# Kernel tuning notes

Hardware: AMD Instinct MI355X
Metric: run time of the kernel (lower is better)

Reference implementation:

```python
import jax, jax.numpy as jnp
import numpy as np

B, N = 2, 6
C_IN, C_MID = 512, 512
D, C_OUT = 112, 80
OGH, OGW, DS = 256, 704, 16
FH, FW = OGH // DS, OGW // DS  # 16, 44
D_MIN, D_MAX = 2.0, 58.0
NX, NY, NZ = 128, 128, 1
VSIZE = np.array([0.8, 0.8, 8.0], dtype=np.float32)
VCOORD = np.array([-51.2 + 0.4, -51.2 + 0.4, -5.0 + 4.0], dtype=np.float32)


def make_frustum():
    # (D, FH, FW, 4) with entries (x_pix, y_pix, depth, 1)
    ones = jnp.ones((D, FH, FW), jnp.float32)
    d = jnp.linspace(D_MIN, D_MAX, D)[:, None, None] * jnp.ones((1, FH, FW))
    x = jnp.linspace(0.0, OGW - 1.0, FW)[None, None, :] * jnp.ones((D, FH, 1))
    y = jnp.linspace(0.0, OGH - 1.0, FH)[None, :, None] * jnp.ones((D, 1, FW))
    return jnp.stack([x, y, d, ones], axis=-1)


def setup_inputs() -> dict:
    key = jax.random.key(0)
    ks = jax.random.split(key, 24)
    eye = jnp.eye(4, dtype=jnp.float32)
    K = jnp.array([[1266.0, 0.0, 800.0, 0.0],
                   [0.0, 1266.0, 450.0, 0.0],
                   [0.0, 0.0, 1.0, 0.0],
                   [0.0, 0.0, 0.0, 1.0]], jnp.float32)
    inp = {
        'feat': jax.random.normal(ks[0], (B * N, C_IN, FH, FW), jnp.float32),
        'w1': 0.05 * jax.random.normal(ks[1], (C_MID, C_IN, 3, 3), jnp.float32),
        'g1': 1.0 + 0.1 * jax.random.normal(ks[2], (C_MID,), jnp.float32),
        'b1': 0.1 * jax.random.normal(ks[3], (C_MID,), jnp.float32),
        'm1': 0.1 * jax.random.normal(ks[4], (C_MID,), jnp.float32),
        'v1': 0.5 + jax.random.uniform(ks[5], (C_MID,), jnp.float32),
        'w2': 0.05 * jax.random.normal(ks[6], (C_MID, C_MID, 3, 3), jnp.float32),
        'g2': 1.0 + 0.1 * jax.random.normal(ks[7], (C_MID,), jnp.float32),
        'b2': 0.1 * jax.random.normal(ks[8], (C_MID,), jnp.float32),
        'm2': 0.1 * jax.random.normal(ks[9], (C_MID,), jnp.float32),
        'v2': 0.5 + jax.random.uniform(ks[10], (C_MID,), jnp.float32),
        'w_out': 0.05 * jax.random.normal(ks[11], (D + C_OUT, C_MID, 1, 1), jnp.float32),
        'b_out': 0.1 * jax.random.normal(ks[12], (D + C_OUT,), jnp.float32),
        'sensor2ego': eye + 0.05 * jax.random.normal(ks[13], (B, N, 4, 4), jnp.float32),
        'sensor2virtual': eye + 0.05 * jax.random.normal(ks[14], (B, N, 4, 4), jnp.float32),
        'intrin': K + 0.01 * jax.random.normal(ks[15], (B, N, 4, 4), jnp.float32),
        'ida': eye + 0.01 * jax.random.normal(ks[16], (B, N, 4, 4), jnp.float32),
        'ref_heights': 1.5 + 0.2 * jax.random.normal(ks[17], (B, N), jnp.float32),
        'bda': eye + 0.01 * jax.random.normal(ks[18], (B, 4, 4), jnp.float32),
    }
    return inp


def _conv(x, w, p):
    return jax.lax.conv_general_dilated(x, w, (1, 1), [(p, p), (p, p)],
                                         dimension_numbers=('NCHW', 'OIHW', 'NCHW'))


def _bn(x, g, b, m, v):
    s = (g / jnp.sqrt(v + 1e-5))
    return (x - m[None, :, None, None]) * s[None, :, None, None] + b[None, :, None, None]


def get_geometry(sensor2ego, sensor2virtual, intrin, ida, ref_heights, bda):
    frustum = make_frustum()[..., None]  # (D,FH,FW,4,1)
    pts = jnp.linalg.inv(ida)[:, :, None, None, None] @ frustum  # (B,N,D,FH,FW,4,1)
    ref = ref_heights[:, :, None, None, None, None]
    height = -pts[..., 2, :] + ref  # (B,N,D,FH,FW,1)
    pc = pts.at[..., 2, :].set(10.0)
    pc = jnp.concatenate([pc[..., :2, :] * pc[..., 2:3, :], pc[..., 2:, :]], axis=-2)
    cv = sensor2virtual @ jnp.linalg.inv(intrin)
    pv = cv[:, :, None, None, None] @ pc
    ratio = height[..., 0] / pv[..., 1, 0]  # (B,N,D,FH,FW)
    pts = pv * ratio[..., None, None]
    pts = pts.at[..., 3, :].set(1.0)
    ce = sensor2ego @ jnp.linalg.inv(sensor2virtual)
    pts = ce[:, :, None, None, None] @ pts
    pts = (bda[:, None, None, None, None] @ pts)[..., 0]
    return pts[..., :3]  # (B,N,D,FH,FW,3)


def reference(feat, w1, g1, b1, m1, v1, w2, g2, b2, m2, v2, w_out, b_out,
              sensor2ego, sensor2virtual, intrin, ida, ref_heights, bda):
    # DepthNet head
    h = jax.nn.relu(_bn(_conv(feat, w1, 1), g1, b1, m1, v1))
    h = jax.nn.relu(_bn(_conv(h, w2, 1), g2, b2, m2, v2))
    hf = _conv(h, w_out, 0) + b_out[None, :, None, None]  # (B*N, D+C, FH, FW)
    depth = jax.nn.softmax(hf[:, :D], axis=1).reshape(B, N, D, FH, FW)
    context = hf[:, D:].reshape(B, N, C_OUT, FH, FW)

    geom = get_geometry(sensor2ego, sensor2virtual, intrin, ida, ref_heights, bda)

    # voxel indices
    vsize = jnp.asarray(VSIZE)
    vcoord = jnp.asarray(VCOORD)
    idx = ((geom - (vcoord - vsize / 2.0)) / vsize).astype(jnp.int32)
    valid = (jnp.all(idx >= 0, axis=-1) & (idx[..., 0] < NX)
             & (idx[..., 1] < NY) & (idx[..., 2] < NZ))

    # LSS outer product: (B,N,D,FH,FW,C)
    vol = jnp.einsum('bndhw,bnchw->bndhwc', depth, context)
    YX = NY * NX
    sid = idx[..., 1] * NX + idx[..., 0] + jnp.arange(B, dtype=jnp.int32)[:, None, None, None, None] * YX
    sid = jnp.where(valid, sid, B * YX).reshape(-1)
    bev = jax.ops.segment_sum(vol.reshape(-1, C_OUT), sid, num_segments=B * YX + 1)[:B * YX]
    return bev.reshape(B, NY, NX, C_OUT).transpose(0, 3, 1, 2)  # (B,C,NY,NX)
```

## Files before the change

kernel.cpp:

```cpp
#include <hip/hip_runtime.h>
#include <stdint.h>

#define NB   2
#define NN   6
#define NIMG 12
#define CIN  512
#define CMID 512
#define DD   112
#define COUT 80
#define FHh  16
#define FWw  44
#define NPIX 704
#define NPOS 8448
#define KK   4608
#define NXg  128
#define NYg  128
#define YX   16384
#define MAT_STRIDE 56
#define PADPIX 828
#define PROW 46

typedef short short8 __attribute__((ext_vector_type(8)));
typedef float f32x4  __attribute__((ext_vector_type(4)));

#define GLD16(g, l) __builtin_amdgcn_global_load_lds((const __attribute__((address_space(1))) void*)(g), (__attribute__((address_space(3))) void*)(l), 16, 0, 0)

__device__ __forceinline__ unsigned short f2bf(float f){
  unsigned u = __float_as_uint(f);
  u += 0x7fffu + ((u >> 16) & 1u);
  return (unsigned short)(u >> 16);
}
__device__ __forceinline__ float bf2f(unsigned short u){
  return __uint_as_float(((unsigned)u) << 16);
}

__device__ __forceinline__ f32x4 mfma16(short8 a, short8 b, f32x4 c){
  return __builtin_amdgcn_mfma_f32_16x16x32_bf16(a, b, c, 0, 0, 0);
}

#define N1 (CMID*KK)
__global__ void k_prep_misc(const float* __restrict__ w1, const float* __restrict__ w2,
                            const float* __restrict__ wout,
                            const float* __restrict__ g1, const float* __restrict__ b1,
                            const float* __restrict__ m1, const float* __restrict__ v1,
                            const float* __restrict__ g2, const float* __restrict__ b2,
                            const float* __restrict__ m2, const float* __restrict__ v2,
                            unsigned short* __restrict__ wb1, unsigned short* __restrict__ wb2,
                            unsigned short* __restrict__ wb3,
                            float* __restrict__ scale1, float* __restrict__ bias1,
                            float* __restrict__ scale2, float* __restrict__ bias2){
  int i = blockIdx.x*blockDim.x + threadIdx.x;
  if (i < 2*N1){
    const float* w = (i < N1) ? w1 : w2;
    unsigned short* wb = (i < N1) ? wb1 : wb2;
    int j = (i < N1) ? i : i - N1;
    int oc = j / KK; int jj = j - oc*KK;
    int r = jj >> 9; int ic = jj & 511;
    wb[j] = f2bf(w[(size_t)(oc*512 + ic)*9 + r]);
  } else if (i < 2*N1 + 192*CMID){
    int j = i - 2*N1;
    wb3[j] = f2bf(wout[j]);
  } else if (i < 2*N1 + 192*CMID + 512){
    int t = i - (2*N1 + 192*CMID);
    float s = g1[t] / sqrtf(v1[t] + 1e-5f);
    scale1[t] = s; bias1[t] = b1[t] - m1[t]*s;
  } else if (i < 2*N1 + 192*CMID + 1024){
    int t = i - (2*N1 + 192*CMID + 512);
    float s = g2[t] / sqrtf(v2[t] + 1e-5f);
    scale2[t] = s; bias2[t] = b2[t] - m2[t]*s;
  }
}

__global__ void k_zeropad(unsigned short* __restrict__ a, unsigned short* __restrict__ b,
                          float4* __restrict__ bev){
  int i = blockIdx.x*blockDim.x + threadIdx.x;
  if (i < NB*YX*COUT/4) bev[i] = make_float4(0.f,0.f,0.f,0.f);
  int img = i >> 16; int j = i & 65535;
  int seg = j >> 9, ch = j & 511;
  int pp;
  if (seg < 46)       pp = seg;
  else if (seg < 92)  pp = 17*PROW + (seg - 46);
  else { int s2 = seg - 92; int y = s2 >> 1; pp = y*PROW + ((s2 & 1) ? 45 : 0); }
  size_t off = (size_t)img*PADPIX*512 + (size_t)pp*512 + ch;
  a[off] = 0; b[off] = 0;
}

__global__ __launch_bounds__(256) void k_featpad(const float* __restrict__ feat,
                                                 unsigned short* __restrict__ dst){
  __shared__ float tile[32][65];
  int blk = blockIdx.x;
  int img = blk / 176; int r = blk - img*176;
  int cb = r / 11; int pb = r - cb*11;
  int c0 = cb*32, p0 = pb*64;
  int t = threadIdx.x;
  const float* s = feat + (size_t)img*CIN*NPIX + (size_t)c0*NPIX + p0;
  for (int ch = t>>6; ch < 32; ch += 4)
    tile[ch][t & 63] = s[(size_t)ch*NPIX + (t & 63)];
  __syncthreads();
  int ch = (t & 15)*2;
  for (int pix = t>>4; pix < 64; pix += 16){
    int p = p0 + pix;
    int y = p / FWw, x = p - y*FWw;
    unsigned v = (unsigned)f2bf(tile[ch][pix]) | ((unsigned)f2bf(tile[ch+1][pix]) << 16);
    *(unsigned*)(dst + (size_t)img*PADPIX*512 + ((y+1)*PROW + (x+1))*512 + c0 + ch) = v;
  }
}

__device__ void inv4(const double* A, double* out){
  double M[4][8];
  for (int i=0;i<4;i++){ for(int j=0;j<4;j++){ M[i][j]=A[i*4+j]; M[i][4+j]=(i==j)?1.0:0.0; } }
  for (int c=0;c<4;c++){
    int piv=c; double best=fabs(M[c][c]);
    for (int r=c+1;r<4;r++){ double a=fabs(M[r][c]); if(a>best){best=a;piv=r;} }
    if (piv!=c){ for(int j=0;j<8;j++){ double tt=M[c][j]; M[c][j]=M[piv][j]; M[piv][j]=tt; } }
    double inv = 1.0 / M[c][c];
    for (int j=0;j<8;j++) M[c][j]*=inv;
    for (int r=0;r<4;r++){ if(r==c) continue; double f=M[r][c];
      for (int j=0;j<8;j++) M[r][j]-=f*M[c][j]; }
  }
  for (int i=0;i<4;i++) for(int j=0;j<4;j++) out[i*4+j]=M[i][4+j];
}
__device__ void mm4(const double* A, const double* Bm, double* C){
  for (int i=0;i<4;i++) for(int j=0;j<4;j++){
    double s=0.0; for(int k=0;k<4;k++) s+=A[i*4+k]*Bm[k*4+j]; C[i*4+j]=s; }
}

__global__ void k_prep_mats(const float* __restrict__ s2e, const float* __restrict__ s2v,
                            const float* __restrict__ intr, const float* __restrict__ ida,
                            const float* __restrict__ refh, const float* __restrict__ bda,
                            double* __restrict__ mats){
  int t = threadIdx.x;
  if (t >= NIMG) return;
  int b = t / NN;
  double Mida[16], Ms2v[16], Mintr[16], Ms2e[16], Mbda[16];
  for (int i=0;i<16;i++){
    Mida[i] =(double)ida [t*16+i];
    Ms2v[i] =(double)s2v [t*16+i];
    Mintr[i]=(double)intr[t*16+i];
    Ms2e[i] =(double)s2e [t*16+i];
    Mbda[i] =(double)bda [b*16+i];
  }
  double* o = mats + (size_t)t*MAT_STRIDE;
  double tmp[16], tmp2[16];
  inv4(Mida, o);
  inv4(Mintr, tmp);  mm4(Ms2v, tmp, o+16);
  inv4(Ms2v, tmp);   mm4(Ms2e, tmp, tmp2);
  mm4(Mbda, tmp2, o+32);
  o[48] = (double)refh[t];
}

__global__ void k_geom(const double* __restrict__ mats, int* __restrict__ sid){
  int g = blockIdx.x*blockDim.x + threadIdx.x;
  int img = g / (DD*NPIX); int rem = g - img*(DD*NPIX);
  int d = rem / NPIX; int p = rem - d*NPIX;
  int h = p / FWw; int w = p - h*FWw;
  const double* M = mats + (size_t)img*MAT_STRIDE;
  float xf = (float)w * (703.0f/43.0f);
  float yf = (float)h * 17.0f;
  float df = 2.0f + (float)d * (56.0f/111.0f);
  double x = (double)xf, y = (double)yf, dep = (double)df;
  double p0 = M[0]*x + M[1]*y + M[2]*dep + M[3];
  double p1 = M[4]*x + M[5]*y + M[6]*dep + M[7];
  double p2 = M[8]*x + M[9]*y + M[10]*dep + M[11];
  double p3 = M[12]*x + M[13]*y + M[14]*dep + M[15];
  double height = M[48] - p2;
  double c0 = p0*10.0, c1 = p1*10.0, c2 = 10.0, c3 = p3;
  const double* C = M + 16;
  double q0 = C[0]*c0 + C[1]*c1 + C[2]*c2 + C[3]*c3;
  double q1 = C[4]*c0 + C[5]*c1 + C[6]*c2 + C[7]*c3;
  double q2 = C[8]*c0 + C[9]*c1 + C[10]*c2 + C[11]*c3;
  double ratio = height / q1;
  double r0 = q0*ratio, r1 = q1*ratio, r2 = q2*ratio, r3 = 1.0;
  const double* F = M + 32;
  double gx = F[0]*r0 + F[1]*r1 + F[2]*r2 + F[3]*r3;
  double gy = F[4]*r0 + F[5]*r1 + F[6]*r2 + F[7]*r3;
  double gz = F[8]*r0 + F[9]*r1 + F[10]*r2 + F[11]*r3;
  float gxf = (float)gx, gyf = (float)gy, gzf = (float)gz;
  const float vcx = (float)(-51.2 + 0.4);
  const float ox = vcx - 0.4f;
  const float oy = ox;
  const float oz = -1.0f - 4.0f;
  float tx = (gxf - ox) / 0.8f;
  float ty = (gyf - oy) / 0.8f;
  float tz = (gzf - oz) / 8.0f;
  int ix = (int)tx, iy = (int)ty, iz = (int)tz;
  bool valid = (tx==tx) && (ty==ty) && (tz==tz) &&
               (ix >= 0) && (ix < NXg) && (iy >= 0) && (iy < NYg) && (iz == 0);
  int b = img / NN;
  sid[g] = valid ? (b*YX + iy*NXg + ix) : -1;
}

__global__ __launch_bounds__(256, 4) void k_conv_sk(const unsigned short* __restrict__ W,
    const unsigned short* __restrict__ src, unsigned short* __restrict__ part,
    int ksplit, int kchunk, int nstep){
  __shared__ __align__(16) short As[2][128*32];
  __shared__ __align__(16) short Bs[2][128*32];
  int t = threadIdx.x;
  int lane = t & 63, wv = t >> 6;
  int wm = wv >> 1, wn = wv & 1;
  int q = lane >> 4, ml = lane & 15;

  int id = blockIdx.x;
  int res = id & 7, slot = id >> 3;
  int g = res + 8*(slot >> 2);
  int mblk = slot & 3;
  int z = g / 66, n = g - z*66;
  int m0 = mblk*128, n0 = n*128, k0 = z*kchunk;

  int lrow = lane >> 2;
  int lcol = (lane & 3) * 8;
  const unsigned short* agp[2];
  const unsigned short* bgp[2];
  #pragma unroll
  for (int i=0;i<2;i++){
    int seg = wv*2 + i;
    agp[i] = W + (size_t)(m0 + seg*16 + lrow)*KK + lcol;
    int pos = n0 + seg*16 + lrow;
    int img = pos / NPIX; int p = pos - img*NPIX;
    int y = p / FWw; int x = p - y*FWw;
    bgp[i] = src + (size_t)img*PADPIX*512 + ((y+1)*PROW + (x+1))*512 + lcol;
  }

  f32x4 acc[4][4];
  #pragma unroll
  for (int i=0;i<4;i++)
    #pragma unroll
    for (int j=0;j<4;j++) acc[i][j] = (f32x4)0.0f;

  auto stage = [&](int step){
    int kb = k0 + step*32;
    int d = step & 1;
    int r = kb >> 9;
    int ic0 = kb & 511;
    int r3 = r / 3;
    int koff = (r3*PROW + (r - r3*3))*512 + ic0 - (PROW+1)*512;
    #pragma unroll
    for (int i=0;i<2;i++){
      int seg = wv*2 + i;
      GLD16(agp[i] + kb,   (char*)As[d] + seg*1024);
      GLD16(bgp[i] + koff, (char*)Bs[d] + seg*1024);
    }
  };

  stage(0);
  for (int k = 0; k < nstep; ++k){
    if (k + 1 < nstep){
      stage(k + 1);
      asm volatile("s_waitcnt vmcnt(4)" ::: "memory");
    } else {
      asm volatile("s_waitcnt vmcnt(0)" ::: "memory");
    }
    asm volatile("s_barrier" ::: "memory");
    const short* Ab = As[k & 1];
    const short* Bb = Bs[k & 1];
    short8 fa[4], fb[4];
    #pragma unroll
    for (int mi=0;mi<4;mi++) fa[mi] = *(const short8*)(Ab + (wm*64 + mi*16 + ml)*32 + q*8);
    #pragma unroll
    for (int ni=0;ni<4;ni++) fb[ni] = *(const short8*)(Bb + (wn*64 + ni*16 + ml)*32 + q*8);
    #pragma unroll
    for (int mi=0;mi<4;mi++)
      #pragma unroll
      for (int ni=0;ni<4;ni++)
        acc[mi][ni] = mfma16(fb[ni], fa[mi], acc[mi][ni]);
    asm volatile("s_barrier" ::: "memory");
  }

  unsigned short* op = part + (size_t)z*NPOS*CMID;
  #pragma unroll
  for (int mi=0;mi<4;mi++){
    int oc = m0 + wm*64 + mi*16 + ml;
    #pragma unroll
    for (int ni=0;ni<4;ni++){
      f32x4 v = acc[mi][ni];
      #pragma unroll
      for (int rr=0;rr<4;rr++){
        int pos = n0 + wn*64 + ni*16 + q*4 + rr;
        op[(size_t)pos*CMID + oc] = f2bf(v[rr]);
      }
    }
  }
}

template<int OUT_PADDED>
__global__ void k_reduce(const unsigned short* __restrict__ part,
                         const float* __restrict__ scale, const float* __restrict__ bias,
                         unsigned short* __restrict__ out, int ksplit){
  int i2 = blockIdx.x*blockDim.x + threadIdx.x;
  int e0 = i2*2;
  const size_t S = (size_t)NPOS*CMID;
  float s0 = 0.0f, s1 = 0.0f;
  for (int z = 0; z < ksplit; ++z){
    unsigned pz = *(const unsigned*)(part + e0 + (size_t)z*S);
    s0 += bf2f((unsigned short)pz);
    s1 += bf2f((unsigned short)(pz >> 16));
  }
  int pos = e0 >> 9, oc = e0 & 511;
  float v0 = fmaxf(s0*scale[oc]   + bias[oc],   0.0f);
  float v1 = fmaxf(s1*scale[oc+1] + bias[oc+1], 0.0f);
  unsigned packed = (unsigned)f2bf(v0) | ((unsigned)f2bf(v1) << 16);
  if (OUT_PADDED){
    int img = pos / NPIX; int p = pos - img*NPIX;
    int y = p / FWw; int x = p - y*FWw;
    *(unsigned*)(out + (size_t)img*PADPIX*512 + ((y+1)*PROW + (x+1))*512 + oc) = packed;
  } else {
    *(unsigned*)(out + e0) = packed;
  }
}

__global__ __launch_bounds__(256) void k_gemm64(const unsigned short* __restrict__ A,
    const unsigned short* __restrict__ Bt, const float* __restrict__ bout,
    float* __restrict__ hf){
  const int K = 512;
  __shared__ __align__(16) short As[2][64*32];
  __shared__ __align__(16) short Bs[2][128*32];
  int t = threadIdx.x;
  int lane = t & 63, wv = t >> 6;
  int q = lane >> 4, ml = lane & 15;
  int m0 = blockIdx.x*64, n0 = blockIdx.y*128;
  int lrow = lane >> 2, lcol = (lane & 3) * 8;
  const unsigned short* agp = A + (size_t)(m0 + wv*16 + lrow)*K + lcol;
  const unsigned short* bgp[2];
  #pragma unroll
  for (int i=0;i<2;i++){
    int seg = wv*2 + i;
    bgp[i] = Bt + (size_t)(n0 + seg*16 + lrow)*K + lcol;
  }
  f32x4 acc[8];
  #pragma unroll
  for (int i=0;i<8;i++) acc[i] = (f32x4)0.0f;

  auto stage = [&](int s){
    int d = s & 1; int kb = s*32;
    GLD16(agp + kb, (char*)As[d] + wv*1024);
    #pragma unroll
    for (int i=0;i<2;i++)
      GLD16(bgp[i] + kb, (char*)Bs[d] + (wv*2+i)*1024);
  };

  stage(0);
  for (int k = 0; k < 16; ++k){
    if (k < 15){
      stage(k + 1);
      asm volatile("s_waitcnt vmcnt(3)" ::: "memory");
    } else {
      asm volatile("s_waitcnt vmcnt(0)" ::: "memory");
    }
    asm volatile("s_barrier" ::: "memory");
    short8 fa = *(const short8*)(As[k & 1] + (wv*16 + ml)*32 + q*8);
    #pragma unroll
    for (int ni=0;ni<8;ni++){
      short8 fb = *(const short8*)(Bs[k & 1] + (ni*16 + ml)*32 + q*8);
      acc[ni] = mfma16(fb, fa, acc[ni]);
    }
    asm volatile("s_barrier" ::: "memory");
  }
  int oc = m0 + wv*16 + ml;
  float bb = bout[oc];
  #pragma unroll
  for (int ni=0;ni<8;ni++)
    #pragma unroll
    for (int r=0;r<4;r++){
      int pos = n0 + ni*16 + q*4 + r;
      hf[(size_t)pos*192 + oc] = acc[ni][r] + bb;
    }
}

__global__ __launch_bounds__(128) void k_scatter(const float* __restrict__ hf,
                          const int* __restrict__ sidb, float* __restrict__ bev){
  int pos = blockIdx.x;
  int img = pos / NPIX; int p = pos - img*NPIX;
  __shared__ float sdep[DD];
  __shared__ int   ssid[DD];
  __shared__ float sctx[COUT];
  __shared__ float cwt[DD];
  __shared__ int   cvox[DD];
  __shared__ int   scnt;
  __shared__ float redm[2];
  __shared__ float reds[2];
  int t = threadIdx.x;
  int wv = t >> 6;
  if (t == 0) scnt = 0;
  const float* row = hf + (size_t)pos*192;
  float v = (t < DD) ? row[t] : -1e30f;
  for (int c = t; c < COUT; c += 128) sctx[c] = row[DD + c];
  if (t < DD) ssid[t] = sidb[(size_t)(img*DD + t)*NPIX + p];
  float m = v;
  #pragma unroll
  for (int o=32;o>=1;o>>=1) m = fmaxf(m, __shfl_xor(m, o, 64));
  if ((t & 63) == 0) redm[wv] = m;
  __syncthreads();
  float mx = fmaxf(redm[0], redm[1]);
  float e = (t < DD) ? __expf(v - mx) : 0.0f;
  float s = e;
  #pragma unroll
  for (int o=32;o>=1;o>>=1) s += __shfl_xor(s, o, 64);
  if ((t & 63) == 0) reds[wv] = s;
  __syncthreads();
  float inv = 1.0f / (reds[0] + reds[1]);
  if (t < DD) sdep[t] = e * inv;
  __syncthreads();
  if (t < DD){
    int sd = ssid[t];
    bool head = (sd >= 0) && (t == 0 || ssid[t-1] != sd);
    if (head){
      float w = 0.0f;
      for (int dd = t; dd < DD && ssid[dd] == sd; ++dd) w += sdep[dd];
      int i = atomicAdd(&scnt, 1);
      cvox[i] = sd; cwt[i] = w;
    }
  }
  __syncthreads();
  int H = scnt;
  for (int j = t; j < H*COUT; j += 128){
    int h = j / COUT, c = j - h*COUT;
    atomicAdd(&bev[(size_t)cvox[h]*COUT + c], cwt[h]*sctx[c]);
  }
}

__global__ __launch_bounds__(256) void k_transpose(const float* __restrict__ bev, float* __restrict__ out){
  __shared__ float tile[64*COUT];
  int blk = blockIdx.x;
  int b = blk >> 8; int yx0 = (blk & 255) * 64;
  int t = threadIdx.x;
  const float* src = bev + ((size_t)b*YX + yx0)*COUT;
  for (int j = t; j < 64*COUT; j += 256) tile[j] = src[j];
  __syncthreads();
  float* dst = out + (size_t)b*COUT*YX + yx0;
  for (int j = t; j < COUT*64; j += 256){
    int c = j >> 6, row = j & 63;
    dst[(size_t)c*YX + row] = tile[row*COUT + c];
  }
}

extern "C" void kernel_launch(void* const* d_in, const int* in_sizes, int n_in,
                              void* d_out, int out_size, void* d_ws, size_t ws_size,
                              hipStream_t stream) {
  const float* feat = (const float*)d_in[0];
  const float* w1   = (const float*)d_in[1];
  const float* g1   = (const float*)d_in[2];
  const float* b1   = (const float*)d_in[3];
  const float* m1   = (const float*)d_in[4];
  const float* v1   = (const float*)d_in[5];
  const float* w2   = (const float*)d_in[6];
  const float* g2   = (const float*)d_in[7];
  const float* b2   = (const float*)d_in[8];
  const float* m2   = (const float*)d_in[9];
  const float* v2   = (const float*)d_in[10];
  const float* wout = (const float*)d_in[11];
  const float* bout = (const float*)d_in[12];
  const float* s2e  = (const float*)d_in[13];
  const float* s2v  = (const float*)d_in[14];
  const float* intr = (const float*)d_in[15];
  const float* ida  = (const float*)d_in[16];
  const float* refh = (const float*)d_in[17];
  const float* bda  = (const float*)d_in[18];

  uint8_t* base = (uint8_t*)d_ws;
  size_t off = 0;
  auto alloc = [&](size_t bytes)->void*{
    void* r = base + off;
    off = (off + bytes + 255) & ~(size_t)255;
    return r;
  };
  unsigned short* wb1 = (unsigned short*)alloc((size_t)CMID*KK*2);
  unsigned short* wb2 = (unsigned short*)alloc((size_t)CMID*KK*2);
  unsigned short* wb3 = (unsigned short*)alloc((size_t)192*CMID*2);
  float* scale1 = (float*)alloc(CMID*4);
  float* bias1  = (float*)alloc(CMID*4);
  float* scale2 = (float*)alloc(CMID*4);
  float* bias2  = (float*)alloc(CMID*4);
  double* mats  = (double*)alloc((size_t)NIMG*MAT_STRIDE*8);

  size_t padded_bytes = (size_t)NIMG*PADPIX*512*2;
  uint8_t* regionE = (uint8_t*)alloc(padded_bytes);
  uint8_t* regionF = (uint8_t*)alloc(padded_bytes);
  int*   sid   = (int*)  alloc((size_t)NIMG*DD*NPIX*4);
  float* bev   = (float*)alloc((size_t)NB*YX*COUT*4);

  size_t slice = (size_t)NPOS*CMID*2;
  size_t rem = (ws_size > off) ? ws_size - off : 0;
  int ksplit = (rem >= 8*slice + 256) ? 8 : 4;
  unsigned short* part = (unsigned short*)alloc((size_t)ksplit*slice);
  int kchunk = KK / ksplit;
  int nstep  = kchunk / 32;

  unsigned short* featpad = (unsigned short*)regionE;
  unsigned short* h2      = (unsigned short*)regionE;
  unsigned short* h1pad   = (unsigned short*)regionF;
  float*          hf      = (float*)regionF;

  int prep_n = 2*N1 + 192*CMID + 1024;
  k_prep_misc<<<(prep_n + 255)/256, 256, 0, stream>>>(w1, w2, wout, g1, b1, m1, v1,
      g2, b2, m2, v2, wb1, wb2, wb3, scale1, bias1, scale2, bias2);
  k_prep_mats<<<1, 64, 0, stream>>>(s2e, s2v, intr, ida, refh, bda, mats);
  k_geom<<<3696, 256, 0, stream>>>(mats, sid);

  k_zeropad<<<3072, 256, 0, stream>>>(featpad, h1pad, (float4*)bev);
  k_featpad<<<2112, 256, 0, stream>>>(feat, featpad);

  k_conv_sk<<<264*ksplit, 256, 0, stream>>>(wb1, featpad, part, ksplit, kchunk, nstep);
  k_reduce<1><<<NPOS*CMID/512, 256, 0, stream>>>(part, scale1, bias1, h1pad, ksplit);
  k_conv_sk<<<264*ksplit, 256, 0, stream>>>(wb2, h1pad, part, ksplit, kchunk, nstep);
  k_reduce<0><<<NPOS*CMID/512, 256, 0, stream>>>(part, scale2, bias2, h2, ksplit);
  k_gemm64<<<dim3(3, 66), 256, 0, stream>>>(wb3, h2, bout, hf);

  k_scatter<<<NPOS, 128, 0, stream>>>(hf, sid, bev);

  k_transpose<<<512, 256, 0, stream>>>(bev, (float*)d_out);
}
```

Measured before the change: 371.9 us.

## Retile conv split-K to 256x64 tiles with weights loaded directly into registers

The 3x3 conv split-K kernel now uses 256(out-channel) x 64(position) tiles, with each wave owning 64 output channels. The weight fragments are loaded straight from global memory into registers, and only the activation tile is staged in LDS, double-buffered with a manually unrolled two-stage loop. The split-K factor is fixed at 4 at compile time, replacing the previous runtime choice between 8 and 4 based on workspace size. The goal is to cut LDS traffic and barrier overhead, at the cost of uncoalesced per-lane weight loads and lower occupancy (launch bounds 3).

Result: slower. 426.7 us (+14.8%).

```diff
diff --git a/kernel.cpp b/kernel.cpp
--- a/kernel.cpp
+++ b/kernel.cpp
@@ -19,6 +19,9 @@
 #define MAT_STRIDE 56
 #define PADPIX 828
 #define PROW 46
+#define KS   4
+#define KCH  (KK/KS)
+#define NST  (KCH/32)
 
 typedef short short8 __attribute__((ext_vector_type(8)));
 typedef float f32x4  __attribute__((ext_vector_type(4)));
@@ -190,36 +193,32 @@
   sid[g] = valid ? (b*YX + iy*NXg + ix) : -1;
 }
 
-__global__ __launch_bounds__(256, 4) void k_conv_sk(const unsigned short* __restrict__ W,
-    const unsigned short* __restrict__ src, unsigned short* __restrict__ part,
-    int ksplit, int kchunk, int nstep){
-  __shared__ __align__(16) short As[2][128*32];
-  __shared__ __align__(16) short Bs[2][128*32];
+__global__ __launch_bounds__(256, 3) void k_conv_sk(const unsigned short* __restrict__ W,
+    const unsigned short* __restrict__ src, unsigned short* __restrict__ part){
+  __shared__ __align__(16) short Bs[2][64*32];
   int t = threadIdx.x;
   int lane = t & 63, wv = t >> 6;
-  int wm = wv >> 1, wn = wv & 1;
   int q = lane >> 4, ml = lane & 15;
 
   int id = blockIdx.x;
   int res = id & 7, slot = id >> 3;
-  int g = res + 8*(slot >> 2);
-  int mblk = slot & 3;
-  int z = g / 66, n = g - z*66;
-  int m0 = mblk*128, n0 = n*128, k0 = z*kchunk;
-
-  int lrow = lane >> 2;
-  int lcol = (lane & 3) * 8;
-  const unsigned short* agp[2];
-  const unsigned short* bgp[2];
-  #pragma unroll
-  for (int i=0;i<2;i++){
-    int seg = wv*2 + i;
-    agp[i] = W + (size_t)(m0 + seg*16 + lrow)*KK + lcol;
-    int pos = n0 + seg*16 + lrow;
-    int img = pos / NPIX; int p = pos - img*NPIX;
-    int y = p / FWw; int x = p - y*FWw;
-    bgp[i] = src + (size_t)img*PADPIX*512 + ((y+1)*PROW + (x+1))*512 + lcol;
-  }
+  int g = res + 8*(slot >> 1);
+  int mblk = slot & 1;
+  int z = g / 132, n = g - z*132;
+  int m0 = mblk*256, n0 = n*64, k0 = z*KCH;
+
+  int brow = t >> 2, bcol = (t & 3)*8;
+  {
+  }
+  int posb = n0 + brow;
+  int imgb = posb / NPIX; int pb = posb - imgb*NPIX;
+  int yb = pb / FWw; int xb = pb - yb*FWw;
+  const unsigned short* bgp = src + (size_t)imgb*PADPIX*512 + ((yb+1)*PROW + (xb+1))*512 + bcol;
+
+  const unsigned short* agp[4];
+  #pragma unroll
+  for (int mi=0;mi<4;mi++)
+    agp[mi] = W + (size_t)(m0 + wv*64 + mi*16 + ml)*KK + k0 + q*8;
 
   f32x4 acc[4][4];
   #pragma unroll
@@ -227,55 +226,67 @@
     #pragma unroll
     for (int j=0;j<4;j++) acc[i][j] = (f32x4)0.0f;
 
-  auto stage = [&](int step){
+  uint4 a0[4], a1[4];
+
+  auto stageB = [&](int step, int d){
     int kb = k0 + step*32;
-    int d = step & 1;
     int r = kb >> 9;
     int ic0 = kb & 511;
     int r3 = r / 3;
     int koff = (r3*PROW + (r - r3*3))*512 + ic0 - (PROW+1)*512;
-    #pragma unroll
-    for (int i=0;i<2;i++){
-      int seg = wv*2 + i;
-      GLD16(agp[i] + kb,   (char*)As[d] + seg*1024);
-      GLD16(bgp[i] + koff, (char*)Bs[d] + seg*1024);
-    }
+    GLD16(bgp + koff, (char*)Bs[d] + wv*1024);
   };
-
-  stage(0);
-  for (int k = 0; k < nstep; ++k){
-    if (k + 1 < nstep){
-      stage(k + 1);
-      asm volatile("s_waitcnt vmcnt(4)" ::: "memory");
+  auto loadA = [&](int step, uint4* ar){
+    int kb = step*32;
+    #pragma unroll
+    for (int mi=0;mi<4;mi++) ar[mi] = *(const uint4*)(agp[mi] + kb);
+  };
+  auto compute = [&](const short* Bp, uint4* ar){
+    short8 fb[4];
+    #pragma unroll
+    for (int ni=0;ni<4;ni++) fb[ni] = *(const short8*)(Bp + (ni*16 + ml)*32 + q*8);
+    #pragma unroll
+    for (int mi=0;mi<4;mi++){
+      short8 fa = *(const short8*)&ar[mi];
+      #pragma unroll
+      for (int ni=0;ni<4;ni++)
+        acc[mi][ni] = mfma16(fb[ni], fa, acc[mi][ni]);
+    }
+  };
+
+  stageB(0, 0);
+  loadA(0, a0);
+  for (int j = 0; j < NST; j += 2){
+    if (j + 1 < NST){
+      stageB(j + 1, 1); loadA(j + 1, a1);
+      asm volatile("s_waitcnt vmcnt(5)" ::: "memory");
     } else {
       asm volatile("s_waitcnt vmcnt(0)" ::: "memory");
     }
     asm volatile("s_barrier" ::: "memory");
-    const short* Ab = As[k & 1];
-    const short* Bb = Bs[k & 1];
-    short8 fa[4], fb[4];
-    #pragma unroll
-    for (int mi=0;mi<4;mi++) fa[mi] = *(const short8*)(Ab + (wm*64 + mi*16 + ml)*32 + q*8);
-    #pragma unroll
-    for (int ni=0;ni<4;ni++) fb[ni] = *(const short8*)(Bb + (wn*64 + ni*16 + ml)*32 + q*8);
-    #pragma unroll
-    for (int mi=0;mi<4;mi++)
-      #pragma unroll
-      for (int ni=0;ni<4;ni++)
-        acc[mi][ni] = mfma16(fb[ni], fa[mi], acc[mi][ni]);
+    compute(Bs[0], a0);
     asm volatile("s_barrier" ::: "memory");
+    if (j + 2 < NST){
+      stageB(j + 2, 0); loadA(j + 2, a0);
+      asm volatile("s_waitcnt vmcnt(5)" ::: "memory");
+    } else {
+      asm volatile("s_waitcnt vmcnt(0)" ::: "memory");
+    }
+    asm volatile("s_barrier" ::: "memory");
+    compute(Bs[1], a1);
+    asm volatile("s_barrier" ::: "memory");
   }
 
   unsigned short* op = part + (size_t)z*NPOS*CMID;
   #pragma unroll
   for (int mi=0;mi<4;mi++){
-    int oc = m0 + wm*64 + mi*16 + ml;
+    int oc = m0 + wv*64 + mi*16 + ml;
     #pragma unroll
     for (int ni=0;ni<4;ni++){
       f32x4 v = acc[mi][ni];
       #pragma unroll
       for (int rr=0;rr<4;rr++){
-        int pos = n0 + wn*64 + ni*16 + q*4 + rr;
+        int pos = n0 + ni*16 + q*4 + rr;
         op[(size_t)pos*CMID + oc] = f2bf(v[rr]);
       }
     }
@@ -285,12 +296,13 @@
 template<int OUT_PADDED>
 __global__ void k_reduce(const unsigned short* __restrict__ part,
                          const float* __restrict__ scale, const float* __restrict__ bias,
-                         unsigned short* __restrict__ out, int ksplit){
+                         unsigned short* __restrict__ out){
   int i2 = blockIdx.x*blockDim.x + threadIdx.x;
   int e0 = i2*2;
   const size_t S = (size_t)NPOS*CMID;
   float s0 = 0.0f, s1 = 0.0f;
-  for (int z = 0; z < ksplit; ++z){
+  #pragma unroll
+  for (int z = 0; z < KS; ++z){
     unsigned pz = *(const unsigned*)(part + e0 + (size_t)z*S);
     s0 += bf2f((unsigned short)pz);
     s1 += bf2f((unsigned short)(pz >> 16));
@@ -477,13 +489,7 @@
   uint8_t* regionF = (uint8_t*)alloc(padded_bytes);
   int*   sid   = (int*)  alloc((size_t)NIMG*DD*NPIX*4);
   float* bev   = (float*)alloc((size_t)NB*YX*COUT*4);
-
-  size_t slice = (size_t)NPOS*CMID*2;
-  size_t rem = (ws_size > off) ? ws_size - off : 0;
-  int ksplit = (rem >= 8*slice + 256) ? 8 : 4;
-  unsigned short* part = (unsigned short*)alloc((size_t)ksplit*slice);
-  int kchunk = KK / ksplit;
-  int nstep  = kchunk / 32;
+  unsigned short* part = (unsigned short*)alloc((size_t)KS*NPOS*CMID*2);
 
   unsigned short* featpad = (unsigned short*)regionE;
   unsigned short* h2      = (unsigned short*)regionE;
@@ -499,10 +505,10 @@
   k_zeropad<<<3072, 256, 0, stream>>>(featpad, h1pad, (float4*)bev);
   k_featpad<<<2112, 256, 0, stream>>>(feat, featpad);
 
-  k_conv_sk<<<264*ksplit, 256, 0, stream>>>(wb1, featpad, part, ksplit, kchunk, nstep);
-  k_reduce<1><<<NPOS*CMID/512, 256, 0, stream>>>(part, scale1, bias1, h1pad, ksplit);
-  k_conv_sk<<<264*ksplit, 256, 0, stream>>>(wb2, h1pad, part, ksplit, kchunk, nstep);
-  k_reduce<0><<<NPOS*CMID/512, 256, 0, stream>>>(part, scale2, bias2, h2, ksplit);
+  k_conv_sk<<<1056, 256, 0, stream>>>(wb1, featpad, part);
+  k_reduce<1><<<NPOS*CMID/512, 256, 0, stream>>>(part, scale1, bias1, h1pad);
+  k_conv_sk<<<1056, 256, 0, stream>>>(wb2, h1pad, part);
+  k_reduce<0><<<NPOS*CMID/512, 256, 0, stream>>>(part, scale2, bias2, h2);
   k_gemm64<<<dim3(3, 66), 256, 0, stream>>>(wb3, h2, bout, hf);
 
   k_scatter<<<NPOS, 128, 0, stream>>>(hf, sid, bev);
```

## Fuse split-K reduction into conv kernel via last-block atomic counter

Applied to the files above, without the earlier changes.

Removes the separate k_reduce launches. Each split-K block now increments a per-tile atomic counter after writing its partial, and the last block to arrive sums all partial slices, applies BN scale/bias and ReLU, and writes the output. This saves two kernel launches and lets the reduction overlap with other tiles' GEMM work. The cost is a serialized reduction tail inside the last block of each tile, and correctness depends on threadfence ordering.

New measurement: 1.195 ms. 221% more time.

```diff
diff --git a/kernel.cpp b/kernel.cpp
--- a/kernel.cpp
+++ b/kernel.cpp
@@ -19,6 +19,7 @@
 #define MAT_STRIDE 56
 #define PADPIX 828
 #define PROW 46
+#define NTILE 264
 
 typedef short short8 __attribute__((ext_vector_type(8)));
 typedef float f32x4  __attribute__((ext_vector_type(4)));
@@ -72,9 +73,10 @@
 }
 
 __global__ void k_zeropad(unsigned short* __restrict__ a, unsigned short* __restrict__ b,
-                          float4* __restrict__ bev){
+                          float4* __restrict__ bev, int* __restrict__ cnt){
   int i = blockIdx.x*blockDim.x + threadIdx.x;
   if (i < NB*YX*COUT/4) bev[i] = make_float4(0.f,0.f,0.f,0.f);
+  if (i < 2*NTILE) cnt[i] = 0;
   int img = i >> 16; int j = i & 65535;
   int seg = j >> 9, ch = j & 511;
   int pp;
@@ -190,11 +192,15 @@
   sid[g] = valid ? (b*YX + iy*NXg + ix) : -1;
 }
 
+template<int OUT_PADDED>
 __global__ __launch_bounds__(256, 4) void k_conv_sk(const unsigned short* __restrict__ W,
     const unsigned short* __restrict__ src, unsigned short* __restrict__ part,
+    const float* __restrict__ scale, const float* __restrict__ bias,
+    unsigned short* __restrict__ out, int* __restrict__ cnt,
     int ksplit, int kchunk, int nstep){
   __shared__ __align__(16) short As[2][128*32];
   __shared__ __align__(16) short Bs[2][128*32];
+  __shared__ int lastflag;
   int t = threadIdx.x;
   int lane = t & 63, wv = t >> 6;
   int wm = wv >> 1, wn = wv & 1;
@@ -280,31 +286,38 @@
       }
     }
   }
-}
-
-template<int OUT_PADDED>
-__global__ void k_reduce(const unsigned short* __restrict__ part,
-                         const float* __restrict__ scale, const float* __restrict__ bias,
-                         unsigned short* __restrict__ out, int ksplit){
-  int i2 = blockIdx.x*blockDim.x + threadIdx.x;
-  int e0 = i2*2;
+
+  __threadfence();
+  if (t == 0){
+    int old = atomicAdd(&cnt[mblk*66 + n], 1);
+    lastflag = (old == ksplit - 1);
+  }
+  __syncthreads();
+  if (!lastflag) return;
+  __threadfence();
+
   const size_t S = (size_t)NPOS*CMID;
-  float s0 = 0.0f, s1 = 0.0f;
-  for (int z = 0; z < ksplit; ++z){
-    unsigned pz = *(const unsigned*)(part + e0 + (size_t)z*S);
-    s0 += bf2f((unsigned short)pz);
-    s1 += bf2f((unsigned short)(pz >> 16));
-  }
-  int pos = e0 >> 9, oc = e0 & 511;
-  float v0 = fmaxf(s0*scale[oc]   + bias[oc],   0.0f);
-  float v1 = fmaxf(s1*scale[oc+1] + bias[oc+1], 0.0f);
-  unsigned packed = (unsigned)f2bf(v0) | ((unsigned)f2bf(v1) << 16);
-  if (OUT_PADDED){
-    int img = pos / NPIX; int p = pos - img*NPIX;
-    int y = p / FWw; int x = p - y*FWw;
-    *(unsigned*)(out + (size_t)img*PADPIX*512 + ((y+1)*PROW + (x+1))*512 + oc) = packed;
-  } else {
-    *(unsigned*)(out + e0) = packed;
+  for (int j = t; j < 8192; j += 256){
+    int prow = j >> 6, opair = j & 63;
+    int pos = n0 + prow;
+    int oc  = m0 + opair*2;
+    size_t e0 = (size_t)pos*CMID + oc;
+    float s0 = 0.0f, s1 = 0.0f;
+    for (int zz = 0; zz < ksplit; ++zz){
+      unsigned pz = *(const unsigned*)(part + e0 + (size_t)zz*S);
+      s0 += bf2f((unsigned short)pz);
+      s1 += bf2f((unsigned short)(pz >> 16));
+    }
+    float v0 = fmaxf(s0*scale[oc]   + bias[oc],   0.0f);
+    float v1 = fmaxf(s1*scale[oc+1] + bias[oc+1], 0.0f);
+    unsigned packed = (unsigned)f2bf(v0) | ((unsigned)f2bf(v1) << 16);
+    if (OUT_PADDED){
+      int img = pos / NPIX; int p = pos - img*NPIX;
+      int y = p / FWw; int x = p - y*FWw;
+      *(unsigned*)(out + (size_t)img*PADPIX*512 + ((y+1)*PROW + (x+1))*512 + oc) = packed;
+    } else {
+      *(unsigned*)(out + e0) = packed;
+    }
   }
 }
 
@@ -471,6 +484,7 @@
   float* scale2 = (float*)alloc(CMID*4);
   float* bias2  = (float*)alloc(CMID*4);
   double* mats  = (double*)alloc((size_t)NIMG*MAT_STRIDE*8);
+  int* cnt      = (int*)alloc(2*NTILE*4);
 
   size_t padded_bytes = (size_t)NIMG*PADPIX*512*2;
   uint8_t* regionE = (uint8_t*)alloc(padded_bytes);
@@ -496,13 +510,13 @@
   k_prep_mats<<<1, 64, 0, stream>>>(s2e, s2v, intr, ida, refh, bda, mats);
   k_geom<<<3696, 256, 0, stream>>>(mats, sid);
 
-  k_zeropad<<<3072, 256, 0, stream>>>(featpad, h1pad, (float4*)bev);
+  k_zeropad<<<3072, 256, 0, stream>>>(featpad, h1pad, (float4*)bev, cnt);
   k_featpad<<<2112, 256, 0, stream>>>(feat, featpad);
 
-  k_conv_sk<<<264*ksplit, 256, 0, stream>>>(wb1, featpad, part, ksplit, kchunk, nstep);
-  k_reduce<1><<<NPOS*CMID/512, 256, 0, stream>>>(part, scale1, bias1, h1pad, ksplit);
-  k_conv_sk<<<264*ksplit, 256, 0, stream>>>(wb2, h1pad, part, ksplit, kchunk, nstep);
-  k_reduce<0><<<NPOS*CMID/512, 256, 0, stream>>>(part, scale2, bias2, h2, ksplit);
+  k_conv_sk<1><<<264*ksplit, 256, 0, stream>>>(wb1, featpad, part, scale1, bias1,
+                                               h1pad, cnt, ksplit, kchunk, nstep);
+  k_conv_sk<0><<<264*ksplit, 256, 0, stream>>>(wb2, h1pad, part, scale2, bias2,
+                                               h2, cnt + NTILE, ksplit, kchunk, nstep);
   k_gemm64<<<dim3(3, 66), 256, 0, stream>>>(wb3, h2, bout, hf);
 
   k_scatter<<<NPOS, 128, 0, stream>>>(hf, sid, bev);
```
